# Kernel optimization log

Hardware: AMD Instinct MI355X
Metric: run time of the kernel (lower is better)

Reference implementation:

```python
import jax, jax.numpy as jnp
import numpy as np

VOCAB = 100000; D = 300; F_NUM = 768
M = 64; N = 16
SURF_L = 4; CTX_L = 50; DOC_L = 100; BODY_L = 200
HEADS = 5


def _conv_relu_avg(x, W, b):
    # x: [B, L, D] tokens-embedded; conv1d (valid) + relu + global avgpool -> [B, F]
    y = jax.lax.conv_general_dilated(x.transpose(0, 2, 1), W, (1,), 'VALID',
                                     dimension_numbers=('NCH', 'OIH', 'NCH'))
    return jax.nn.relu(y + b[None, :, None]).mean(axis=2)


def _mha(q, k, v, num_heads=HEADS):
    # split-head scaled dot-product attention (no learned projections), q:[Lq,D] k,v:[Lk,D]
    Lq, Dm = q.shape
    hd = Dm // num_heads
    qh = q.reshape(Lq, num_heads, hd).transpose(1, 0, 2)
    kh = k.reshape(k.shape[0], num_heads, hd).transpose(1, 0, 2)
    vh = v.reshape(v.shape[0], num_heads, hd).transpose(1, 0, 2)
    att = jax.nn.softmax(jnp.einsum('hqd,hkd->hqk', qh, kh) * (1.0 / np.sqrt(hd)), axis=-1)
    out = jnp.einsum('hqk,hkd->hqd', att, vh)
    return out.transpose(1, 0, 2).reshape(Lq, Dm)


def _cos(a, b, eps=1e-6):
    na = jnp.maximum(jnp.sqrt((a * a).sum(-1)), eps)
    nb = jnp.maximum(jnp.sqrt((b * b).sum(-1)), eps)
    return (a * b).sum(-1) / (na * nb)


def setup_inputs() -> dict:
    key = jax.random.key(0)
    ks = jax.random.split(key, 20)
    inp = {}
    inp['mention_entity'] = jnp.ones((M, N), dtype=jnp.int32)
    inp['m'] = M
    inp['n'] = N
    inp['mention_vec'] = jax.random.randint(ks[0], (M, SURF_L), 0, VOCAB)
    inp['context_vec'] = jax.random.randint(ks[1], (M, CTX_L), 0, VOCAB)
    inp['doc_vec'] = jax.random.randint(ks[2], (DOC_L,), 0, VOCAB)
    inp['title_vec'] = jax.random.normal(ks[3], (N, F_NUM), dtype=jnp.float32)
    inp['body_vec'] = jax.random.randint(ks[4], (N, BODY_L), 0, VOCAB)
    inp['sfeats'] = jnp.zeros((N, 1), dtype=jnp.float32)
    inp['m2c_prior'] = jax.random.uniform(ks[5], (N,), dtype=jnp.float32)
    inp['men2cands'] = jax.random.randint(ks[6], (M, N), 0, VOCAB)
    inp['contexts_ids'] = jax.random.randint(ks[7], (M, CTX_L), 0, VOCAB)
    inp['hand_features'] = jax.random.uniform(ks[8], (N, 1), dtype=jnp.float32)
    inp['bert_doc_vec'] = jax.random.normal(ks[9], (1, F_NUM), dtype=jnp.float32)
    # learned parameters
    inp['embed_table'] = jax.random.normal(ks[10], (VOCAB, D), dtype=jnp.float32) * 0.1
    inp['conv_ms_w'] = jax.random.normal(ks[11], (F_NUM, D, 2), dtype=jnp.float32) * 0.05
    inp['conv_ms_b'] = jnp.zeros((F_NUM,), dtype=jnp.float32)
    inp['conv_mc_w'] = jax.random.normal(ks[12], (F_NUM, D, 5), dtype=jnp.float32) * 0.05
    inp['conv_mc_b'] = jnp.zeros((F_NUM,), dtype=jnp.float32)
    inp['layer_local_w'] = jax.random.normal(ks[13], (7,), dtype=jnp.float32) * 0.3
    inp['layer_local_b'] = jnp.zeros((), dtype=jnp.float32)
    inp['att_w1'] = jax.random.normal(ks[14], (600, 300), dtype=jnp.float32) * 0.05
    inp['att_b1'] = jnp.zeros((300,), dtype=jnp.float32)
    inp['att_w2'] = jax.random.normal(ks[15], (300, 1), dtype=jnp.float32) * 0.05
    inp['att_b2'] = jnp.zeros((), dtype=jnp.float32)
    return inp


def reference(mention_entity, m, n, mention_vec, context_vec, doc_vec, title_vec,
              body_vec, sfeats, m2c_prior, men2cands, contexts_ids, hand_features,
              bert_doc_vec, embed_table, conv_ms_w, conv_ms_b, conv_mc_w, conv_mc_b,
              layer_local_w, layer_local_b, att_w1, att_b1, att_w2, att_b2):
    # per-mention conv features (vectorized over all mentions at once)
    ms = _conv_relu_avg(embed_table[mention_vec], conv_ms_w, conv_ms_b)   # [M,768]
    mc = _conv_relu_avg(embed_table[context_vec], conv_mc_w, conv_mc_b)   # [M,768]
    md = bert_doc_vec[0]                                                  # [768]
    doc_emb = embed_table[doc_vec]                                        # [100,300]
    body_emb = embed_table[body_vec]                                      # [N,200,300]

    # per-candidate cross attention doc<->body, max-pooled over query positions
    att_d_b = jax.vmap(lambda b: _mha(doc_emb, b, b).max(axis=0))(body_emb)          # [N,300]
    att_b_d = jax.vmap(lambda b: _mha(b, doc_emb, doc_emb).max(axis=0))(body_emb)    # [N,300]
    comb = jnp.concatenate([att_d_b, att_b_d], axis=-1)                              # [N,600]
    att_score = jax.nn.sigmoid(jax.nn.relu(comb @ att_w1 + att_b1) @ att_w2 + att_b2)[:, 0]  # [N]

    # LocalCtxAttRanker: candidate-vs-context attention score
    ctx_emb = embed_table[contexts_ids]                                   # [M,50,300]
    cand_emb = embed_table[men2cands]                                     # [M,N,300]
    tok = jnp.einsum('mnd,mtd->mnt', cand_emb, ctx_emb)                   # [M,N,50]
    p = jax.nn.softmax(tok.max(axis=1), axis=-1)                          # [M,50]
    ctxv = jnp.einsum('mt,mtd->md', p, ctx_emb)                           # [M,300]
    local_att = jnp.einsum('mnd,md->mn', cand_emb, ctxv)                  # [M,N]

    cos_st = _cos(ms[:, None, :], title_vec[None, :, :])                  # [M,N]
    cos_dt = _cos(md[None, :], title_vec)                                 # [N]
    cos_ct = _cos(mc[:, None, :], title_vec[None, :, :])                  # [M,N]

    Mm = ms.shape[0]
    bc = lambda v: jnp.broadcast_to(v[None, :], (Mm, v.shape[0]))
    # feature order matches torch.cat((hand_fea, prior, localAtt, attScore, C_score))
    feats = jnp.stack([bc(hand_features[:, 0]), bc(m2c_prior), local_att,
                       bc(att_score), cos_st, bc(cos_dt), cos_ct], axis=-1)  # [M,N,7]
    score = feats @ layer_local_w + layer_local_b                         # [M,N]

    # per-mention standardization (unbiased std, as torch.std), softmax and uniform renorm
    mu = score.mean(axis=1, keepdims=True)
    sd = score.std(axis=1, keepdims=True, ddof=1)
    z = (score - mu) / sd
    sm = jax.nn.softmax(z, axis=1)
    zmin = z.min(axis=1, keepdims=True)
    zmax = z.max(axis=1, keepdims=True)
    u = (z + 1.0 - zmin) / (zmax - zmin)
    u = u / u.sum(axis=1, keepdims=True)
    return (z, sm, u)
```

## Files before the change

kernel.cpp:

```cpp
#include <hip/hip_runtime.h>

#define MM 64
#define NN 16
#define DDIM 300
#define FNUM 768
#define SURF_LL 4
#define CTX_LL 50
#define DOC_LL 100
#define BODY_LL 200
#define NHEADS 5
#define HDIM 60

#define GM 2944
#define GK 1536
#define GN 768

typedef unsigned short u16;
typedef unsigned int u32;
typedef __attribute__((ext_vector_type(8))) short short8;
typedef __attribute__((ext_vector_type(4))) float f32x4;

#define OFF_MSG    0
#define OFF_CTX2G  76800
#define OFF_CANDG  1036800
#define OFF_MS     1344000
#define OFF_MC     1393152
#define OFF_PV0    1442304
#define OFF_PV1    1451904
#define OFF_ASC    1471104
#define OFF_TOKMAX 1471120
#define OFF_LATT   1474320
#define OFF_ABF    1475344
#define OFF_WTMC   (OFF_ABF + GM*GK/2)
#define OFF_WTMS   (OFF_WTMC + GN*GK/2)
#define OFF_P      (OFF_WTMS + 600*768)

__device__ __forceinline__ u16 f2bf(float x) {
  union { float f; u32 u; } v; v.f = x;
  u32 r = v.u + 0x7FFFu + ((v.u >> 16) & 1u);
  return (u16)(r >> 16);
}

__global__ __launch_bounds__(256) void gather_kernel(
    const float* __restrict__ embed,
    const int* __restrict__ mention_vec,
    const int* __restrict__ contexts_ids,
    const int* __restrict__ men2cands,
    float* __restrict__ dst,
    float* __restrict__ mc) {
  int e = blockIdx.x * 256 + threadIdx.x;
  if (e < 1344000) {
    int row = e / DDIM;
    int col = e - row * DDIM;
    int tok;
    if (row < 256)       tok = mention_vec[row];
    else if (row < 3456) tok = contexts_ids[row - 256];
    else                 tok = men2cands[row - 3456];
    dst[e] = embed[(size_t)tok * DDIM + col];
  } else {
    mc[e - 1344000] = 0.f;
  }
}

__global__ __launch_bounds__(256) void prep_kernel(
    const float* __restrict__ embed,
    const int* __restrict__ context_vec,
    const float* __restrict__ Wmc,
    const float* __restrict__ Wms,
    u32* __restrict__ Abf, u32* __restrict__ WTmc, float* __restrict__ WTms) {
  int bid = blockIdx.x;
  if (bid < 8832) {
    int idx = bid * 256 + threadIdx.x;
    int r = idx / (GK / 2);
    int kp = idx - r * (GK / 2);
    int k = kp * 2;
    int m = r / 46, t = r - m * 46;
    u32 out = 0;
#pragma unroll
    for (int j = 0; j < 2; j++) {
      int kj = k + j;
      u16 h = 0;
      if (kj < 1500) {
        int tap = kj / 300;
        int d = kj - tap * 300;
        int tok = context_vec[m * CTX_LL + t + tap];
        h = f2bf(embed[(size_t)tok * DDIM + d]);
      }
      out |= (u32)h << (16 * j);
    }
    Abf[idx] = out;
  } else if (bid < 11136) {
    int idx = (bid - 8832) * 256 + threadIdx.x;
    int n = idx / (GK / 2);
    int kp = idx - n * (GK / 2);
    int k = kp * 2;
    u32 out = 0;
#pragma unroll
    for (int j = 0; j < 2; j++) {
      int kj = k + j;
      u16 h = 0;
      if (kj < 1500) {
        int tap = kj / 300;
        int d = kj - tap * 300;
        h = f2bf(Wmc[(size_t)n * 1500 + d * 5 + tap]);
      }
      out |= (u32)h << (16 * j);
    }
    WTmc[idx] = out;
  } else {
    int idx = (bid - 11136) * 256 + threadIdx.x;
    int k = idx / FNUM;
    int f = idx - k * FNUM;
    WTms[idx] = Wms[(size_t)f * 600 + k];
  }
}

__global__ __launch_bounds__(256) void conv_gemm_kernel(
    const u16* __restrict__ A,
    const u16* __restrict__ B,
    const float* __restrict__ bias,
    float* __restrict__ mc) {
  int bn = blockIdx.x, bm = blockIdx.y;
  __shared__ u16 As[64][72];
  __shared__ u16 Bs[64][72];
  int tid = threadIdx.x;
  int w = tid >> 6, lane = tid & 63;
  int wr = w >> 1, wc = w & 1;
  int lg = lane >> 4, lm = lane & 15;
  f32x4 acc[2][2];
#pragma unroll
  for (int i = 0; i < 2; i++)
#pragma unroll
    for (int j = 0; j < 2; j++) acc[i][j] = (f32x4)0.f;
  int c0row = tid >> 3, ck = (tid & 7) * 8;
  const u16* Ag = A + (size_t)(bm * 64) * GK;
  const u16* Bg = B + (size_t)(bn * 64) * GK;
  for (int kt = 0; kt < GK / 64; kt++) {
    int k0 = kt * 64;
    uint4 av0 = *(const uint4*)(Ag + (size_t)c0row * GK + k0 + ck);
    uint4 av1 = *(const uint4*)(Ag + (size_t)(c0row + 32) * GK + k0 + ck);
    uint4 bv0 = *(const uint4*)(Bg + (size_t)c0row * GK + k0 + ck);
    uint4 bv1 = *(const uint4*)(Bg + (size_t)(c0row + 32) * GK + k0 + ck);
    __syncthreads();
    *(uint4*)&As[c0row][ck] = av0;
    *(uint4*)&As[c0row + 32][ck] = av1;
    *(uint4*)&Bs[c0row][ck] = bv0;
    *(uint4*)&Bs[c0row + 32][ck] = bv1;
    __syncthreads();
#pragma unroll
    for (int kk = 0; kk < 2; kk++) {
      short8 af0 = *(const short8*)&As[wr * 32 + lm][kk * 32 + lg * 8];
      short8 af1 = *(const short8*)&As[wr * 32 + 16 + lm][kk * 32 + lg * 8];
      short8 bf0 = *(const short8*)&Bs[wc * 32 + lm][kk * 32 + lg * 8];
      short8 bf1 = *(const short8*)&Bs[wc * 32 + 16 + lm][kk * 32 + lg * 8];
      acc[0][0] = __builtin_amdgcn_mfma_f32_16x16x32_bf16(af0, bf0, acc[0][0], 0, 0, 0);
      acc[0][1] = __builtin_amdgcn_mfma_f32_16x16x32_bf16(af0, bf1, acc[0][1], 0, 0, 0);
      acc[1][0] = __builtin_amdgcn_mfma_f32_16x16x32_bf16(af1, bf0, acc[1][0], 0, 0, 0);
      acc[1][1] = __builtin_amdgcn_mfma_f32_16x16x32_bf16(af1, bf1, acc[1][1], 0, 0, 0);
    }
  }
#pragma unroll
  for (int mf = 0; mf < 2; mf++)
#pragma unroll
    for (int nf = 0; nf < 2; nf++) {
      int col = bn * 64 + wc * 32 + nf * 16 + lm;
      float bb = bias[col];
      int base = bm * 64 + wr * 32 + mf * 16 + lg * 4;
      int mcur = base / 46;
      float s = 0.f;
#pragma unroll
      for (int r = 0; r < 4; r++) {
        float v = fmaxf(acc[mf][nf][r] + bb, 0.f) * (1.0f / 46.0f);
        int mm = (base + r) / 46;
        if (mm != mcur) { atomicAdd(&mc[mcur * FNUM + col], s); s = 0.f; mcur = mm; }
        s += v;
      }
      atomicAdd(&mc[mcur * FNUM + col], s);
    }
}

__global__ __launch_bounds__(256) void conv_ms_kernel(
    const float* __restrict__ msg,
    const float* __restrict__ WT,
    const float* __restrict__ B,
    float* __restrict__ ms) {
  int m = blockIdx.x;
  int f = blockIdx.y * 256 + threadIdx.x;
  const float* x = msg + m * SURF_LL * DDIM;
  float a0 = 0.f, a1 = 0.f, a2 = 0.f;
  for (int d = 0; d < DDIM; d++) {
    float v0 = x[d], v1 = x[DDIM + d], v2 = x[2 * DDIM + d], v3 = x[3 * DDIM + d];
    float wA = WT[(size_t)(2 * d) * FNUM + f];
    float wB = WT[(size_t)(2 * d + 1) * FNUM + f];
    a0 += v0 * wA + v1 * wB;
    a1 += v1 * wA + v2 * wB;
    a2 += v2 * wA + v3 * wB;
  }
  float b = B[f];
  float r = fmaxf(a0 + b, 0.f) + fmaxf(a1 + b, 0.f) + fmaxf(a2 + b, 0.f);
  ms[m * FNUM + f] = r * (1.0f / 3.0f);
}

template <int DIR>
__global__ __launch_bounds__(256) void attn_scores_kernel(
    const float* __restrict__ embed,
    const int* __restrict__ doc_vec,
    const int* __restrict__ body_vec,
    float* __restrict__ P) {
  constexpr int Lq = DIR ? 200 : 100;
  constexpr int Lk = DIR ? 100 : 200;
  constexpr int KPL = DIR ? 2 : 4;
  int qt = blockIdx.x, n = blockIdx.y, h = blockIdx.z;
  const int* qids = DIR ? body_vec + n * BODY_LL : doc_vec;
  const int* kids = DIR ? doc_vec : body_vec + n * BODY_LL;
  __shared__ float Ks[Lk * 61];
  __shared__ float Qs[32 * 61];
  for (int idx = threadIdx.x; idx < Lk * 15; idx += 256) {
    int r = idx / 15, c = idx - r * 15;
    float4 v = *(const float4*)(embed + (size_t)kids[r] * DDIM + h * HDIM + c * 4);
    float* dp = Ks + r * 61 + c * 4;
    dp[0] = v.x; dp[1] = v.y; dp[2] = v.z; dp[3] = v.w;
  }
  for (int idx = threadIdx.x; idx < 32 * 15; idx += 256) {
    int r = idx / 15, c = idx - r * 15;
    int q = qt * 32 + r; if (q >= Lq) q = Lq - 1;
    float4 v = *(const float4*)(embed + (size_t)qids[q] * DDIM + h * HDIM + c * 4);
    float* dp = Qs + r * 61 + c * 4;
    dp[0] = v.x; dp[1] = v.y; dp[2] = v.z; dp[3] = v.w;
  }
  __syncthreads();
  int w = threadIdx.x >> 6, lane = threadIdx.x & 63;
  float acc[8][KPL];
#pragma unroll
  for (int i = 0; i < 8; i++)
#pragma unroll
    for (int j = 0; j < KPL; j++) acc[i][j] = 0.f;
  for (int d = 0; d < HDIM; d++) {
    float kv[KPL];
#pragma unroll
    for (int j = 0; j < KPL; j++) {
      int kk = lane + 64 * j; if (kk >= Lk) kk = Lk - 1;
      kv[j] = Ks[kk * 61 + d];
    }
#pragma unroll
    for (int i = 0; i < 8; i++) {
      float qv = Qs[(w * 8 + i) * 61 + d];
#pragma unroll
      for (int j = 0; j < KPL; j++) acc[i][j] += qv * kv[j];
    }
  }
  const float scale = 0.12909944487358056f;
#pragma unroll
  for (int i = 0; i < 8; i++) {
    int q = qt * 32 + w * 8 + i;
    float mx = -1e30f;
#pragma unroll
    for (int j = 0; j < KPL; j++)
      if (lane + 64 * j < Lk) mx = fmaxf(mx, acc[i][j]);
#pragma unroll
    for (int o = 32; o >= 1; o >>= 1) mx = fmaxf(mx, __shfl_xor(mx, o));
    float mxs = mx * scale;
    float p[KPL];
    float s = 0.f;
#pragma unroll
    for (int j = 0; j < KPL; j++) {
      p[j] = (lane + 64 * j < Lk) ? __expf(acc[i][j] * scale - mxs) : 0.f;
      s += p[j];
    }
#pragma unroll
    for (int o = 32; o >= 1; o >>= 1) s += __shfl_xor(s, o);
    float inv = 1.0f / s;
    if (q < Lq) {
      float* rowp = P + (size_t)((n * 2 + DIR) * NHEADS + h) * 20000 + q * Lk;
#pragma unroll
      for (int j = 0; j < KPL; j++) {
        int kk = lane + 64 * j;
        if (kk < Lk) rowp[kk] = p[j] * inv;
      }
    }
  }
}

__global__ __launch_bounds__(256) void attn_pv_kernel(
    const float* __restrict__ embed,
    const int* __restrict__ doc_vec,
    const int* __restrict__ body_vec,
    const float* __restrict__ P,
    float* __restrict__ pv0,
    float* __restrict__ pv1) {
  int bid = blockIdx.x;
  int dir, pt, n, h;
  if (bid < 160) { dir = 0; h = bid % 5; n = (bid / 5) % 16; pt = bid / 80; }
  else { int b = bid - 160; dir = 1; h = b % 5; n = (b / 5) % 16; pt = b / 80; }
  int Lq = dir ? 200 : 100;
  int Lk = dir ? 100 : 200;
  int Lk4 = Lk >> 2;
  int K4STR = dir ? 27 : 51;
  const int* kids = dir ? doc_vec : body_vec + n * BODY_LL;
  __shared__ float4 Kt4[60 * 51];
  __shared__ float red[4][64];
  float* Ktf = (float*)Kt4;
  int RS = K4STR * 4;
  for (int idx = threadIdx.x; idx < Lk * 15; idx += 256) {
    int r = idx / 15, c = idx - r * 15;
    float4 v = *(const float4*)(embed + (size_t)kids[r] * DDIM + h * HDIM + c * 4);
    Ktf[(c * 4 + 0) * RS + r] = v.x;
    Ktf[(c * 4 + 1) * RS + r] = v.y;
    Ktf[(c * 4 + 2) * RS + r] = v.z;
    Ktf[(c * 4 + 3) * RS + r] = v.w;
  }
  __syncthreads();
  int lane = threadIdx.x & 63;
  int w = __builtin_amdgcn_readfirstlane(threadIdx.x >> 6);
  int dl = (lane < HDIM) ? lane : (HDIM - 1);
  const float4* Krow = Kt4 + dl * K4STR;
  const float* Pb = P + (size_t)((n * 2 + dir) * NHEADS + h) * 20000;
  float omax = -1e30f;
#pragma unroll
  for (int p = 0; p < 4; p++) {
    int q0 = pt * 64 + p * 16 + w * 4;
    int qa0 = min(q0, Lq - 1), qa1 = min(q0 + 1, Lq - 1);
    int qa2 = min(q0 + 2, Lq - 1), qa3 = min(q0 + 3, Lq - 1);
    const float4* P0 = (const float4*)(Pb + (size_t)qa0 * Lk);
    const float4* P1 = (const float4*)(Pb + (size_t)qa1 * Lk);
    const float4* P2 = (const float4*)(Pb + (size_t)qa2 * Lk);
    const float4* P3 = (const float4*)(Pb + (size_t)qa3 * Lk);
    float o0 = 0.f, o1 = 0.f, o2 = 0.f, o3 = 0.f;
    for (int k4 = 0; k4 < Lk4; k4++) {
      float4 pp0 = P0[k4], pp1 = P1[k4], pp2 = P2[k4], pp3 = P3[k4];
      float4 kk = Krow[k4];
      o0 += pp0.x * kk.x + pp0.y * kk.y + pp0.z * kk.z + pp0.w * kk.w;
      o1 += pp1.x * kk.x + pp1.y * kk.y + pp1.z * kk.z + pp1.w * kk.w;
      o2 += pp2.x * kk.x + pp2.y * kk.y + pp2.z * kk.z + pp2.w * kk.w;
      o3 += pp3.x * kk.x + pp3.y * kk.y + pp3.z * kk.z + pp3.w * kk.w;
    }
    if (q0 < Lq)     omax = fmaxf(omax, o0);
    if (q0 + 1 < Lq) omax = fmaxf(omax, o1);
    if (q0 + 2 < Lq) omax = fmaxf(omax, o2);
    if (q0 + 3 < Lq) omax = fmaxf(omax, o3);
  }
  red[threadIdx.x >> 6][lane] = omax;
  __syncthreads();
  if (threadIdx.x < 64 && lane < HDIM) {
    float m4 = fmaxf(fmaxf(red[0][lane], red[1][lane]),
                     fmaxf(red[2][lane], red[3][lane]));
    float* dst = dir ? pv1 + (size_t)((n * NHEADS + h) * 4 + pt) * HDIM
                     : pv0 + (size_t)((n * NHEADS + h) * 2 + pt) * HDIM;
    dst[lane] = m4;
  }
}

__global__ __launch_bounds__(256) void mlp_kernel(
    const float* __restrict__ pv0, const float* __restrict__ pv1,
    const float* __restrict__ w1, const float* __restrict__ b1,
    const float* __restrict__ w2, const float* __restrict__ b2,
    float* __restrict__ att_score) {
  int n = blockIdx.x, tid = threadIdx.x;
  __shared__ float comb[600];
  for (int idx = tid; idx < 300; idx += 256) {
    int h = idx / 60, d = idx - h * 60;
    float mx = -1e30f;
#pragma unroll
    for (int pt = 0; pt < 2; pt++)
      mx = fmaxf(mx, pv0[(size_t)((n * NHEADS + h) * 2 + pt) * HDIM + d]);
    comb[idx] = mx;
    mx = -1e30f;
#pragma unroll
    for (int pt = 0; pt < 4; pt++)
      mx = fmaxf(mx, pv1[(size_t)((n * NHEADS + h) * 4 + pt) * HDIM + d]);
    comb[300 + idx] = mx;
  }
  __syncthreads();
  float partial = 0.f;
  for (int j = tid; j < 300; j += 256) {
    float hh = b1[j];
    for (int k = 0; k < 600; k++) hh += comb[k] * w1[k * 300 + j];
    partial += fmaxf(hh, 0.f) * w2[j];
  }
  __shared__ float redd[256];
  redd[tid] = partial;
  __syncthreads();
  for (int s = 128; s > 0; s >>= 1) {
    if (tid < s) redd[tid] += redd[tid + s];
    __syncthreads();
  }
  if (tid == 0) att_score[n] = 1.0f / (1.0f + expf(-(redd[0] + b2[0])));
}

__global__ __launch_bounds__(256) void tok_kernel(
    const float* __restrict__ candg,
    const float* __restrict__ ctx2g,
    float* __restrict__ tokmax) {
  int m = blockIdx.x;
  __shared__ float cand[NN * DDIM];
  __shared__ float ctx[16 * DDIM];
  __shared__ float tokb[NN][17];
  for (int i = threadIdx.x; i < NN * DDIM; i += 256)
    cand[i] = candg[(size_t)m * NN * DDIM + i];
  int nI = threadIdx.x >> 4, tt = threadIdx.x & 15;
  for (int cb2 = 0; cb2 < 2; cb2++) {
    int cbase = blockIdx.y * 32 + cb2 * 16;
    __syncthreads();
    for (int i = threadIdx.x; i < 16 * DDIM; i += 256) {
      int rr = i / DDIM, cc = i - rr * DDIM;
      int t = cbase + rr;
      ctx[rr * DDIM + cc] = (t < CTX_LL) ? ctx2g[(size_t)(m * CTX_LL + t) * DDIM + cc] : 0.f;
    }
    __syncthreads();
    const float4* ca = (const float4*)(cand + nI * DDIM);
    const float4* cb = (const float4*)(ctx + tt * DDIM);
    float dsum = 0.f;
#pragma unroll
    for (int c = 0; c < 75; c++) {
      float4 a = ca[c], b = cb[c];
      dsum += a.x * b.x + a.y * b.y + a.z * b.z + a.w * b.w;
    }
    tokb[nI][tt] = dsum;
    __syncthreads();
    if (threadIdx.x < 16) {
      float mx = -1e30f;
      for (int nn = 0; nn < NN; nn++) mx = fmaxf(mx, tokb[nn][threadIdx.x]);
      int t = cbase + threadIdx.x;
      if (t < CTX_LL) tokmax[m * CTX_LL + t] = mx;
    }
  }
}

__global__ __launch_bounds__(256) void ctxv_kernel(
    const float* __restrict__ tokmax,
    const float* __restrict__ ctx2g,
    const float* __restrict__ candg,
    float* __restrict__ local_att) {
  int m = blockIdx.x, tid = threadIdx.x;
  __shared__ float p[64];
  __shared__ float sctxv[DDIM];
  if (tid < 64) {
    float v = (tid < CTX_LL) ? tokmax[m * CTX_LL + tid] : -1e30f;
    float mx = v;
#pragma unroll
    for (int o = 32; o >= 1; o >>= 1) mx = fmaxf(mx, __shfl_xor(mx, o));
    float e = (tid < CTX_LL) ? expf(v - mx) : 0.f;
    float s = e;
#pragma unroll
    for (int o = 32; o >= 1; o >>= 1) s += __shfl_xor(s, o);
    p[tid] = e / s;
  }
  __syncthreads();
  for (int d = tid; d < DDIM; d += 256) {
    float acc = 0.f;
    for (int t = 0; t < CTX_LL; t++)
      acc += p[t] * ctx2g[(size_t)(m * CTX_LL + t) * DDIM + d];
    sctxv[d] = acc;
  }
  __syncthreads();
  int nI = tid >> 4, j = tid & 15;
  float dd = 0.f;
  for (int i = j; i < DDIM; i += 16)
    dd += candg[(size_t)(m * NN + nI) * DDIM + i] * sctxv[i];
#pragma unroll
  for (int o = 8; o >= 1; o >>= 1) dd += __shfl_xor(dd, o);
  if (j == 0) local_att[m * NN + nI] = dd;
}

__global__ __launch_bounds__(256) void final_kernel(
    const float* __restrict__ ms,
    const float* __restrict__ mc,
    const float* __restrict__ title,
    const float* __restrict__ bert,
    const float* __restrict__ att_score,
    const float* __restrict__ m2c_prior,
    const float* __restrict__ hand,
    const float* __restrict__ local_att,
    const float* __restrict__ w7,
    const float* __restrict__ b7,
    float* __restrict__ out) {
  int m = blockIdx.x, tid = threadIdx.x;
  __shared__ float sms[FNUM], smc[FNUM], smd[FNUM];
  __shared__ float snorm[3], sscore[16], wred[3][4];
  for (int i = tid; i < FNUM; i += 256) {
    sms[i] = ms[m * FNUM + i];
    smc[i] = mc[m * FNUM + i];
    smd[i] = bert[i];
  }
  __syncthreads();
  float p1 = 0.f, p2 = 0.f, p3 = 0.f;
  for (int i = tid; i < FNUM; i += 256) {
    float a = sms[i], b = smc[i], c = smd[i];
    p1 += a * a; p2 += b * b; p3 += c * c;
  }
#pragma unroll
  for (int o = 32; o >= 1; o >>= 1) {
    p1 += __shfl_xor(p1, o); p2 += __shfl_xor(p2, o); p3 += __shfl_xor(p3, o);
  }
  int wid = tid >> 6, lane = tid & 63;
  if (lane == 0) { wred[0][wid] = p1; wred[1][wid] = p2; wred[2][wid] = p3; }
  __syncthreads();
  if (tid == 0) {
    snorm[0] = fmaxf(sqrtf(wred[0][0] + wred[0][1] + wred[0][2] + wred[0][3]), 1e-6f);
    snorm[1] = fmaxf(sqrtf(wred[1][0] + wred[1][1] + wred[1][2] + wred[1][3]), 1e-6f);
    snorm[2] = fmaxf(sqrtf(wred[2][0] + wred[2][1] + wred[2][2] + wred[2][3]), 1e-6f);
  }
  __syncthreads();
  int nI = tid >> 4, j = tid & 15;
  float d1 = 0.f, d2 = 0.f, d3 = 0.f, d4 = 0.f;
  for (int i = j; i < FNUM; i += 16) {
    float t = title[nI * FNUM + i];
    d1 += sms[i] * t; d2 += smc[i] * t; d3 += smd[i] * t; d4 += t * t;
  }
#pragma unroll
  for (int o = 8; o >= 1; o >>= 1) {
    d1 += __shfl_xor(d1, o); d2 += __shfl_xor(d2, o);
    d3 += __shfl_xor(d3, o); d4 += __shfl_xor(d4, o);
  }
  if (j == 0) {
    float nt = fmaxf(sqrtf(d4), 1e-6f);
    float cos_st = d1 / (snorm[0] * nt);
    float cos_ct = d2 / (snorm[1] * nt);
    float cos_dt = d3 / (snorm[2] * nt);
    float score = hand[nI] * w7[0] + m2c_prior[nI] * w7[1] +
                  local_att[m * NN + nI] * w7[2] + att_score[nI] * w7[3] +
                  cos_st * w7[4] + cos_dt * w7[5] + cos_ct * w7[6] + b7[0];
    sscore[nI] = score;
  }
  __syncthreads();
  if (tid < 16) {
    float x = sscore[tid];
    float s = x;
#pragma unroll
    for (int o = 8; o >= 1; o >>= 1) s += __shfl_xor(s, o);
    float mu = s * (1.0f / 16.0f);
    float dv = (x - mu) * (x - mu);
    float vs = dv;
#pragma unroll
    for (int o = 8; o >= 1; o >>= 1) vs += __shfl_xor(vs, o);
    float sd = sqrtf(vs * (1.0f / 15.0f));
    float z = (x - mu) / sd;
    float zm = z;
#pragma unroll
    for (int o = 8; o >= 1; o >>= 1) zm = fmaxf(zm, __shfl_xor(zm, o));
    float e = expf(z - zm);
    float es = e;
#pragma unroll
    for (int o = 8; o >= 1; o >>= 1) es += __shfl_xor(es, o);
    float sm = e / es;
    float zmin = z;
#pragma unroll
    for (int o = 8; o >= 1; o >>= 1) zmin = fminf(zmin, __shfl_xor(zmin, o));
    float u0 = (z + 1.0f - zmin) / (zm - zmin);
    float us = u0;
#pragma unroll
    for (int o = 8; o >= 1; o >>= 1) us += __shfl_xor(us, o);
    float u = u0 / us;
    out[m * NN + tid] = z;
    out[MM * NN + m * NN + tid] = sm;
    out[2 * MM * NN + m * NN + tid] = u;
  }
}

extern "C" void kernel_launch(void* const* d_in, const int* in_sizes, int n_in,
                              void* d_out, int out_size, void* d_ws, size_t ws_size,
                              hipStream_t stream) {
  const int*   mention_vec   = (const int*)d_in[3];
  const int*   context_vec   = (const int*)d_in[4];
  const int*   doc_vec       = (const int*)d_in[5];
  const float* title_vec     = (const float*)d_in[6];
  const int*   body_vec      = (const int*)d_in[7];
  const float* m2c_prior     = (const float*)d_in[9];
  const int*   men2cands     = (const int*)d_in[10];
  const int*   contexts_ids  = (const int*)d_in[11];
  const float* hand_features = (const float*)d_in[12];
  const float* bert_doc_vec  = (const float*)d_in[13];
  const float* embed_table   = (const float*)d_in[14];
  const float* conv_ms_w     = (const float*)d_in[15];
  const float* conv_ms_b     = (const float*)d_in[16];
  const float* conv_mc_w     = (const float*)d_in[17];
  const float* conv_mc_b     = (const float*)d_in[18];
  const float* layer_local_w = (const float*)d_in[19];
  const float* layer_local_b = (const float*)d_in[20];
  const float* att_w1        = (const float*)d_in[21];
  const float* att_b1        = (const float*)d_in[22];
  const float* att_w2        = (const float*)d_in[23];
  const float* att_b2        = (const float*)d_in[24];

  float* ws     = (float*)d_ws;
  float* msg    = ws + OFF_MSG;
  float* ctx2g  = ws + OFF_CTX2G;
  float* candg  = ws + OFF_CANDG;
  float* ms     = ws + OFF_MS;
  float* mc     = ws + OFF_MC;
  float* pv0    = ws + OFF_PV0;
  float* pv1    = ws + OFF_PV1;
  float* att_sc = ws + OFF_ASC;
  float* tokmax = ws + OFF_TOKMAX;
  float* latt   = ws + OFF_LATT;
  u16*   Abf    = (u16*)(ws + OFF_ABF);
  u16*   WTmc   = (u16*)(ws + OFF_WTMC);
  float* WTms   = ws + OFF_WTMS;
  float* P      = ws + OFF_P;
  float* out    = (float*)d_out;

  gather_kernel<<<dim3(5442), dim3(256), 0, stream>>>(
      embed_table, mention_vec, contexts_ids, men2cands, ws, mc);
  prep_kernel<<<dim3(12936), dim3(256), 0, stream>>>(
      embed_table, context_vec, conv_mc_w, conv_ms_w, (u32*)Abf, (u32*)WTmc, WTms);
  conv_gemm_kernel<<<dim3(GN / 64, GM / 64), dim3(256), 0, stream>>>(
      Abf, WTmc, conv_mc_b, mc);
  conv_ms_kernel<<<dim3(MM, 3), dim3(256), 0, stream>>>(msg, WTms, conv_ms_b, ms);
  attn_scores_kernel<0><<<dim3(4, NN, NHEADS), dim3(256), 0, stream>>>(
      embed_table, doc_vec, body_vec, P);
  attn_scores_kernel<1><<<dim3(7, NN, NHEADS), dim3(256), 0, stream>>>(
      embed_table, doc_vec, body_vec, P);
  attn_pv_kernel<<<dim3(480), dim3(256), 0, stream>>>(
      embed_table, doc_vec, body_vec, P, pv0, pv1);
  mlp_kernel<<<dim3(NN), dim3(256), 0, stream>>>(pv0, pv1, att_w1, att_b1, att_w2, att_b2, att_sc);
  tok_kernel<<<dim3(MM, 2), dim3(256), 0, stream>>>(candg, ctx2g, tokmax);
  ctxv_kernel<<<dim3(MM), dim3(256), 0, stream>>>(tokmax, ctx2g, candg, latt);
  final_kernel<<<dim3(MM), dim3(256), 0, stream>>>(
      ms, mc, title_vec, bert_doc_vec, att_sc, m2c_prior, hand_features,
      latt, layer_local_w, layer_local_b, out);
}
```

Before: 459.1 us.

## Merge prep and mid-stage kernels into combined launches; vectorize attention score loads

Merges the gather and prep kernels into one launch, and merges conv_ms, both attention-score directions and the tok/ctxv pair into one block-indexed kernel with shared scratch memory. tok and ctxv are fused per mention, so the tokmax workspace round-trip disappears. The attention score inner loop is re-padded to strides of 62 and 64 and uses float2/float4 shared loads. This aims to cut launch overhead and serialization between small independent kernels. The cost is a large shared allocation for every block, including conv_ms blocks that use none of it, which can lower occupancy, and a tok stage that now runs on half as many blocks.

After: 417.6 us (median of 2 runs). 1.1x faster.

```diff
diff --git a/kernel.cpp b/kernel.cpp
--- a/kernel.cpp
+++ b/kernel.cpp
@@ -28,9 +28,8 @@
 #define OFF_PV0    1442304
 #define OFF_PV1    1451904
 #define OFF_ASC    1471104
-#define OFF_TOKMAX 1471120
-#define OFF_LATT   1474320
-#define OFF_ABF    1475344
+#define OFF_LATT   1471120
+#define OFF_ABF    1472144
 #define OFF_WTMC   (OFF_ABF + GM*GK/2)
 #define OFF_WTMS   (OFF_WTMC + GN*GK/2)
 #define OFF_P      (OFF_WTMS + 600*768)
@@ -41,15 +40,19 @@
   return (u16)(r >> 16);
 }
 
-__global__ __launch_bounds__(256) void gather_kernel(
+__global__ __launch_bounds__(256) void mega_prep_kernel(
     const float* __restrict__ embed,
     const int* __restrict__ mention_vec,
+    const int* __restrict__ context_vec,
     const int* __restrict__ contexts_ids,
     const int* __restrict__ men2cands,
-    float* __restrict__ dst,
-    float* __restrict__ mc) {
-  int e = blockIdx.x * 256 + threadIdx.x;
-  if (e < 1344000) {
+    const float* __restrict__ Wmc,
+    const float* __restrict__ Wms,
+    float* __restrict__ dst, float* __restrict__ mc,
+    u32* __restrict__ Abf, u32* __restrict__ WTmc, float* __restrict__ WTms) {
+  int bid = blockIdx.x;
+  if (bid < 5250) {
+    int e = bid * 256 + threadIdx.x;
     int row = e / DDIM;
     int col = e - row * DDIM;
     int tok;
@@ -57,20 +60,10 @@
     else if (row < 3456) tok = contexts_ids[row - 256];
     else                 tok = men2cands[row - 3456];
     dst[e] = embed[(size_t)tok * DDIM + col];
-  } else {
-    mc[e - 1344000] = 0.f;
-  }
-}
-
-__global__ __launch_bounds__(256) void prep_kernel(
-    const float* __restrict__ embed,
-    const int* __restrict__ context_vec,
-    const float* __restrict__ Wmc,
-    const float* __restrict__ Wms,
-    u32* __restrict__ Abf, u32* __restrict__ WTmc, float* __restrict__ WTms) {
-  int bid = blockIdx.x;
-  if (bid < 8832) {
-    int idx = bid * 256 + threadIdx.x;
+  } else if (bid < 5442) {
+    mc[(bid - 5250) * 256 + threadIdx.x] = 0.f;
+  } else if (bid < 14274) {
+    int idx = (bid - 5442) * 256 + threadIdx.x;
     int r = idx / (GK / 2);
     int kp = idx - r * (GK / 2);
     int k = kp * 2;
@@ -89,8 +82,8 @@
       out |= (u32)h << (16 * j);
     }
     Abf[idx] = out;
-  } else if (bid < 11136) {
-    int idx = (bid - 8832) * 256 + threadIdx.x;
+  } else if (bid < 16578) {
+    int idx = (bid - 14274) * 256 + threadIdx.x;
     int n = idx / (GK / 2);
     int kp = idx - n * (GK / 2);
     int k = kp * 2;
@@ -108,7 +101,7 @@
     }
     WTmc[idx] = out;
   } else {
-    int idx = (bid - 11136) * 256 + threadIdx.x;
+    int idx = (bid - 16578) * 256 + threadIdx.x;
     int k = idx / FNUM;
     int f = idx - k * FNUM;
     WTms[idx] = Wms[(size_t)f * 600 + k];
@@ -179,13 +172,11 @@
     }
 }
 
-__global__ __launch_bounds__(256) void conv_ms_kernel(
-    const float* __restrict__ msg,
-    const float* __restrict__ WT,
-    const float* __restrict__ B,
-    float* __restrict__ ms) {
-  int m = blockIdx.x;
-  int f = blockIdx.y * 256 + threadIdx.x;
+__device__ __forceinline__ void conv_ms_body(
+    const float* __restrict__ msg, const float* __restrict__ WT,
+    const float* __restrict__ B, float* __restrict__ ms, int b) {
+  int m = b / 3, fi = b - m * 3;
+  int f = fi * 256 + threadIdx.x;
   const float* x = msg + m * SURF_LL * DDIM;
   float a0 = 0.f, a1 = 0.f, a2 = 0.f;
   for (int d = 0; d < DDIM; d++) {
@@ -196,57 +187,65 @@
     a1 += v1 * wA + v2 * wB;
     a2 += v2 * wA + v3 * wB;
   }
-  float b = B[f];
-  float r = fmaxf(a0 + b, 0.f) + fmaxf(a1 + b, 0.f) + fmaxf(a2 + b, 0.f);
+  float bb = B[f];
+  float r = fmaxf(a0 + bb, 0.f) + fmaxf(a1 + bb, 0.f) + fmaxf(a2 + bb, 0.f);
   ms[m * FNUM + f] = r * (1.0f / 3.0f);
 }
 
 template <int DIR>
-__global__ __launch_bounds__(256) void attn_scores_kernel(
-    const float* __restrict__ embed,
-    const int* __restrict__ doc_vec,
-    const int* __restrict__ body_vec,
-    float* __restrict__ P) {
+__device__ __forceinline__ void scores_body(
+    const float* __restrict__ embed, const int* __restrict__ doc_vec,
+    const int* __restrict__ body_vec, float* __restrict__ P, int b,
+    float* __restrict__ smem) {
   constexpr int Lq = DIR ? 200 : 100;
   constexpr int Lk = DIR ? 100 : 200;
   constexpr int KPL = DIR ? 2 : 4;
-  int qt = blockIdx.x, n = blockIdx.y, h = blockIdx.z;
+  int qt = b / 80;
+  int rem = b - qt * 80;
+  int n = rem / 5, h = rem - n * 5;
   const int* qids = DIR ? body_vec + n * BODY_LL : doc_vec;
   const int* kids = DIR ? doc_vec : body_vec + n * BODY_LL;
-  __shared__ float Ks[Lk * 61];
-  __shared__ float Qs[32 * 61];
+  float* Ks = smem;
+  float* Qs = smem + Lk * 62;
   for (int idx = threadIdx.x; idx < Lk * 15; idx += 256) {
     int r = idx / 15, c = idx - r * 15;
     float4 v = *(const float4*)(embed + (size_t)kids[r] * DDIM + h * HDIM + c * 4);
-    float* dp = Ks + r * 61 + c * 4;
+    float* dp = Ks + r * 62 + c * 4;
     dp[0] = v.x; dp[1] = v.y; dp[2] = v.z; dp[3] = v.w;
   }
   for (int idx = threadIdx.x; idx < 32 * 15; idx += 256) {
     int r = idx / 15, c = idx - r * 15;
     int q = qt * 32 + r; if (q >= Lq) q = Lq - 1;
     float4 v = *(const float4*)(embed + (size_t)qids[q] * DDIM + h * HDIM + c * 4);
-    float* dp = Qs + r * 61 + c * 4;
+    float* dp = Qs + r * 64 + c * 4;
     dp[0] = v.x; dp[1] = v.y; dp[2] = v.z; dp[3] = v.w;
   }
   __syncthreads();
   int w = threadIdx.x >> 6, lane = threadIdx.x & 63;
+  int kcl[KPL];
+#pragma unroll
+  for (int j = 0; j < KPL; j++) {
+    int kk = lane + 64 * j; kcl[j] = (kk < Lk) ? kk : (Lk - 1);
+  }
   float acc[8][KPL];
 #pragma unroll
   for (int i = 0; i < 8; i++)
 #pragma unroll
     for (int j = 0; j < KPL; j++) acc[i][j] = 0.f;
-  for (int d = 0; d < HDIM; d++) {
-    float kv[KPL];
+  for (int d = 0; d < HDIM; d += 4) {
+    float2 kva[KPL], kvb[KPL];
 #pragma unroll
     for (int j = 0; j < KPL; j++) {
-      int kk = lane + 64 * j; if (kk >= Lk) kk = Lk - 1;
-      kv[j] = Ks[kk * 61 + d];
+      kva[j] = *(const float2*)&Ks[kcl[j] * 62 + d];
+      kvb[j] = *(const float2*)&Ks[kcl[j] * 62 + d + 2];
     }
 #pragma unroll
     for (int i = 0; i < 8; i++) {
-      float qv = Qs[(w * 8 + i) * 61 + d];
-#pragma unroll
-      for (int j = 0; j < KPL; j++) acc[i][j] += qv * kv[j];
+      float4 qv = *(const float4*)&Qs[(w * 8 + i) * 64 + d];
+#pragma unroll
+      for (int j = 0; j < KPL; j++)
+        acc[i][j] += qv.x * kva[j].x + qv.y * kva[j].y +
+                     qv.z * kvb[j].x + qv.w * kvb[j].y;
     }
   }
   const float scale = 0.12909944487358056f;
@@ -278,6 +277,98 @@
         if (kk < Lk) rowp[kk] = p[j] * inv;
       }
     }
+  }
+}
+
+__device__ __forceinline__ void tokctxv_body(
+    const float* __restrict__ candg, const float* __restrict__ ctx2g,
+    float* __restrict__ local_att, int m, float* __restrict__ smem) {
+  float* cand  = smem;
+  float* ctx   = smem + 4800;
+  float* tokb  = smem + 9600;
+  float* tkmx  = smem + 9872;
+  float* pp    = smem + 9936;
+  float* sctxv = smem + 10000;
+  int tid = threadIdx.x;
+  for (int i = tid; i < NN * DDIM; i += 256)
+    cand[i] = candg[(size_t)m * NN * DDIM + i];
+  int nI = tid >> 4, tt = tid & 15;
+  for (int tile = 0; tile < 4; tile++) {
+    int cbase = tile * 16;
+    __syncthreads();
+    for (int i = tid; i < 16 * DDIM; i += 256) {
+      int rr = i / DDIM, cc = i - rr * DDIM;
+      int t = cbase + rr;
+      ctx[rr * DDIM + cc] = (t < CTX_LL) ? ctx2g[(size_t)(m * CTX_LL + t) * DDIM + cc] : 0.f;
+    }
+    __syncthreads();
+    const float4* ca = (const float4*)(cand + nI * DDIM);
+    const float4* cb = (const float4*)(ctx + tt * DDIM);
+    float dsum = 0.f;
+#pragma unroll
+    for (int c = 0; c < 75; c++) {
+      float4 a = ca[c], b = cb[c];
+      dsum += a.x * b.x + a.y * b.y + a.z * b.z + a.w * b.w;
+    }
+    tokb[nI * 17 + tt] = dsum;
+    __syncthreads();
+    if (tid < 16) {
+      float mx = -1e30f;
+      for (int nn = 0; nn < NN; nn++) mx = fmaxf(mx, tokb[nn * 17 + tid]);
+      int t = cbase + tid;
+      if (t < CTX_LL) tkmx[t] = mx;
+    }
+  }
+  __syncthreads();
+  if (tid < 64) {
+    float v = (tid < CTX_LL) ? tkmx[tid] : -1e30f;
+    float mx = v;
+#pragma unroll
+    for (int o = 32; o >= 1; o >>= 1) mx = fmaxf(mx, __shfl_xor(mx, o));
+    float e = (tid < CTX_LL) ? expf(v - mx) : 0.f;
+    float s = e;
+#pragma unroll
+    for (int o = 32; o >= 1; o >>= 1) s += __shfl_xor(s, o);
+    pp[tid] = e / s;
+  }
+  __syncthreads();
+  for (int d = tid; d < DDIM; d += 256) {
+    float acc = 0.f;
+    for (int t = 0; t < CTX_LL; t++)
+      acc += pp[t] * ctx2g[(size_t)(m * CTX_LL + t) * DDIM + d];
+    sctxv[d] = acc;
+  }
+  __syncthreads();
+  int j = tid & 15;
+  float dd = 0.f;
+  for (int i = j; i < DDIM; i += 16) dd += cand[nI * DDIM + i] * sctxv[i];
+#pragma unroll
+  for (int o = 8; o >= 1; o >>= 1) dd += __shfl_xor(dd, o);
+  if (j == 0) local_att[m * NN + nI] = dd;
+}
+
+__global__ __launch_bounds__(256) void mega_mid_kernel(
+    const float* __restrict__ embed,
+    const int* __restrict__ doc_vec,
+    const int* __restrict__ body_vec,
+    const float* __restrict__ msg,
+    const float* __restrict__ WTms,
+    const float* __restrict__ Bms,
+    const float* __restrict__ candg,
+    const float* __restrict__ ctx2g,
+    float* __restrict__ ms,
+    float* __restrict__ P,
+    float* __restrict__ local_att) {
+  __shared__ float smem[14448];
+  int bid = blockIdx.x;
+  if (bid < 192) {
+    conv_ms_body(msg, WTms, Bms, ms, bid);
+  } else if (bid < 512) {
+    scores_body<0>(embed, doc_vec, body_vec, P, bid - 192, smem);
+  } else if (bid < 1072) {
+    scores_body<1>(embed, doc_vec, body_vec, P, bid - 512, smem);
+  } else {
+    tokctxv_body(candg, ctx2g, local_att, bid - 1072, smem);
   }
 }
 
@@ -387,81 +478,6 @@
   if (tid == 0) att_score[n] = 1.0f / (1.0f + expf(-(redd[0] + b2[0])));
 }
 
-__global__ __launch_bounds__(256) void tok_kernel(
-    const float* __restrict__ candg,
-    const float* __restrict__ ctx2g,
-    float* __restrict__ tokmax) {
-  int m = blockIdx.x;
-  __shared__ float cand[NN * DDIM];
-  __shared__ float ctx[16 * DDIM];
-  __shared__ float tokb[NN][17];
-  for (int i = threadIdx.x; i < NN * DDIM; i += 256)
-    cand[i] = candg[(size_t)m * NN * DDIM + i];
-  int nI = threadIdx.x >> 4, tt = threadIdx.x & 15;
-  for (int cb2 = 0; cb2 < 2; cb2++) {
-    int cbase = blockIdx.y * 32 + cb2 * 16;
-    __syncthreads();
-    for (int i = threadIdx.x; i < 16 * DDIM; i += 256) {
-      int rr = i / DDIM, cc = i - rr * DDIM;
-      int t = cbase + rr;
-      ctx[rr * DDIM + cc] = (t < CTX_LL) ? ctx2g[(size_t)(m * CTX_LL + t) * DDIM + cc] : 0.f;
-    }
-    __syncthreads();
-    const float4* ca = (const float4*)(cand + nI * DDIM);
-    const float4* cb = (const float4*)(ctx + tt * DDIM);
-    float dsum = 0.f;
-#pragma unroll
-    for (int c = 0; c < 75; c++) {
-      float4 a = ca[c], b = cb[c];
-      dsum += a.x * b.x + a.y * b.y + a.z * b.z + a.w * b.w;
-    }
-    tokb[nI][tt] = dsum;
-    __syncthreads();
-    if (threadIdx.x < 16) {
-      float mx = -1e30f;
-      for (int nn = 0; nn < NN; nn++) mx = fmaxf(mx, tokb[nn][threadIdx.x]);
-      int t = cbase + threadIdx.x;
-      if (t < CTX_LL) tokmax[m * CTX_LL + t] = mx;
-    }
-  }
-}
-
-__global__ __launch_bounds__(256) void ctxv_kernel(
-    const float* __restrict__ tokmax,
-    const float* __restrict__ ctx2g,
-    const float* __restrict__ candg,
-    float* __restrict__ local_att) {
-  int m = blockIdx.x, tid = threadIdx.x;
-  __shared__ float p[64];
-  __shared__ float sctxv[DDIM];
-  if (tid < 64) {
-    float v = (tid < CTX_LL) ? tokmax[m * CTX_LL + tid] : -1e30f;
-    float mx = v;
-#pragma unroll
-    for (int o = 32; o >= 1; o >>= 1) mx = fmaxf(mx, __shfl_xor(mx, o));
-    float e = (tid < CTX_LL) ? expf(v - mx) : 0.f;
-    float s = e;
-#pragma unroll
-    for (int o = 32; o >= 1; o >>= 1) s += __shfl_xor(s, o);
-    p[tid] = e / s;
-  }
-  __syncthreads();
-  for (int d = tid; d < DDIM; d += 256) {
-    float acc = 0.f;
-    for (int t = 0; t < CTX_LL; t++)
-      acc += p[t] * ctx2g[(size_t)(m * CTX_LL + t) * DDIM + d];
-    sctxv[d] = acc;
-  }
-  __syncthreads();
-  int nI = tid >> 4, j = tid & 15;
-  float dd = 0.f;
-  for (int i = j; i < DDIM; i += 16)
-    dd += candg[(size_t)(m * NN + nI) * DDIM + i] * sctxv[i];
-#pragma unroll
-  for (int o = 8; o >= 1; o >>= 1) dd += __shfl_xor(dd, o);
-  if (j == 0) local_att[m * NN + nI] = dd;
-}
-
 __global__ __launch_bounds__(256) void final_kernel(
     const float* __restrict__ ms,
     const float* __restrict__ mc,
@@ -591,7 +607,6 @@
   float* pv0    = ws + OFF_PV0;
   float* pv1    = ws + OFF_PV1;
   float* att_sc = ws + OFF_ASC;
-  float* tokmax = ws + OFF_TOKMAX;
   float* latt   = ws + OFF_LATT;
   u16*   Abf    = (u16*)(ws + OFF_ABF);
   u16*   WTmc   = (u16*)(ws + OFF_WTMC);
@@ -599,22 +614,17 @@
   float* P      = ws + OFF_P;
   float* out    = (float*)d_out;
 
-  gather_kernel<<<dim3(5442), dim3(256), 0, stream>>>(
-      embed_table, mention_vec, contexts_ids, men2cands, ws, mc);
-  prep_kernel<<<dim3(12936), dim3(256), 0, stream>>>(
-      embed_table, context_vec, conv_mc_w, conv_ms_w, (u32*)Abf, (u32*)WTmc, WTms);
+  mega_prep_kernel<<<dim3(18378), dim3(256), 0, stream>>>(
+      embed_table, mention_vec, context_vec, contexts_ids, men2cands,
+      conv_mc_w, conv_ms_w, ws, mc, (u32*)Abf, (u32*)WTmc, WTms);
   conv_gemm_kernel<<<dim3(GN / 64, GM / 64), dim3(256), 0, stream>>>(
       Abf, WTmc, conv_mc_b, mc);
-  conv_ms_kernel<<<dim3(MM, 3), dim3(256), 0, stream>>>(msg, WTms, conv_ms_b, ms);
-  attn_scores_kernel<0><<<dim3(4, NN, NHEADS), dim3(256), 0, stream>>>(
-      embed_table, doc_vec, body_vec, P);
-  attn_scores_kernel<1><<<dim3(7, NN, NHEADS), dim3(256), 0, stream>>>(
-      embed_table, doc_vec, body_vec, P);
+  mega_mid_kernel<<<dim3(1136), dim3(256), 0, stream>>>(
+      embed_table, doc_vec, body_vec, msg, WTms, conv_ms_b, candg, ctx2g,
+      ms, P, latt);
   attn_pv_kernel<<<dim3(480), dim3(256), 0, stream>>>(
       embed_table, doc_vec, body_vec, P, pv0, pv1);
   mlp_kernel<<<dim3(NN), dim3(256), 0, stream>>>(pv0, pv1, att_w1, att_b1, att_w2, att_b2, att_sc);
-  tok_kernel<<<dim3(MM, 2), dim3(256), 0, stream>>>(candg, ctx2g, tokmax);
-  ctxv_kernel<<<dim3(MM), dim3(256), 0, stream>>>(tokmax, ctx2g, candg, latt);
   final_kernel<<<dim3(MM), dim3(256), 0, stream>>>(
       ms, mc, title_vec, bert_doc_vec, att_sc, m2c_prior, hand_features,
       latt, layer_local_w, layer_local_b, out);
```
